# Kernel tuning notes

Measured on AMD Instinct MI355X. Metric: run time of the kernel, lower is better.

The kernel has to match this reference:

```python
import jax, jax.numpy as jnp
import numpy as np

SAMPLE_SIZE = 8192
K = 8
N_SPLATS = 1_000_000
EPS = 1e-12  # keeps sqrt grad finite on zero-distance (duplicate) pairs


def setup_inputs() -> dict:
    key = jax.random.key(0)
    k1, k2, k3 = jax.random.split(key, 3)
    means = jax.random.normal(k1, (N_SPLATS, 3), dtype=jnp.float32)
    sh0 = jax.random.normal(k2, (N_SPLATS, 1, 3), dtype=jnp.float32)
    idx = jax.random.randint(k3, (SAMPLE_SIZE,), 0, N_SPLATS, dtype=jnp.int64)
    return {"means": means, "sh0": sh0, "idx": idx}


def reference(means, sh0, idx):
    sh0 = sh0.squeeze(1)                    # [N, 3]
    sm = means[idx]                         # [S, 3] sampled positions
    ss = sh0[idx]                           # [S, 3] sampled colors
    # pairwise euclidean distances (torch.cdist, p=2): [S, S]
    sq = jnp.sum(sm * sm, axis=-1)
    d2 = sq[:, None] + sq[None, :] - 2.0 * (sm @ sm.T)
    dist = jnp.sqrt(jnp.maximum(d2, EPS))
    # k+1 smallest per row; drop self (column 0)
    _, knn_idx = jax.lax.top_k(-dist, K + 1)           # [S, K+1]
    knn_idx = knn_idx[:, 1:]                           # [S, K]
    neighbors_sh0 = ss[knn_idx]                        # [S, K, 3]
    neighbor_dist = jnp.take_along_axis(dist, knn_idx, axis=1)[..., None]  # [S, K, 1]
    weight = jnp.exp(-neighbor_dist)
    diff = ss[:, None, :] - neighbors_sh0              # [S, K, 3]
    return jnp.mean(weight * diff * diff)
```

## Files before the change

### kernel.cpp

```cpp
#include <hip/hip_runtime.h>
#include <float.h>
#include <math.h>

#define NSAMPLE 8192
#define KSEL 9
#define KNN 8
#define BLK 512
#define EPS_F 1e-12f

#define ROWS_PB 8
#define NBLOCKS (NSAMPLE / ROWS_PB)
#define RPT 8
#define LANES 64
#define KQT 16
#define CHUNK 128
#define NCHUNK (1024 / CHUNK)
#define BNDI 4
#define WCAP 32
#define BP 129
#define IDX_MASK 0x1FFFu
#define VAL_MASK 0xFFFFE000u
#define PROW 73
#define SROW 145
#define SCALE (1.0f / (float)(NSAMPLE * KNN * 3))

__device__ __forceinline__ unsigned umn(unsigned a, unsigned b) { return a < b ? a : b; }
__device__ __forceinline__ unsigned umx(unsigned a, unsigned b) { return a > b ? a : b; }

__device__ __forceinline__ void insert9(unsigned s[KSEL], unsigned x)
{
#pragma unroll
    for (int k = 0; k < KSEL - 1; ++k)
        s[k] = umx(s[k + 1], umn(x, s[k]));
    s[KSEL - 1] = umn(x, s[KSEL - 1]);
}

__device__ __forceinline__ unsigned pack_d2(float d2, int gidx)
{
    return (__float_as_uint(fmaxf(d2, 0.0f)) & VAL_MASK) | (unsigned)gidx;
}

__device__ __forceinline__ float sfl(float x)
{
    return __uint_as_float((unsigned)__builtin_amdgcn_readfirstlane(
        (int)__float_as_uint(x)));
}

__device__ __forceinline__ unsigned mbcnt64(unsigned long long m)
{
    return __builtin_amdgcn_mbcnt_hi((unsigned)(m >> 32),
           __builtin_amdgcn_mbcnt_lo((unsigned)(m & 0xFFFFFFFFull), 0u));
}

__device__ __forceinline__ void load_lds16(const float4* g, float4* l)
{
    __builtin_amdgcn_global_load_lds(
        (const __attribute__((address_space(1))) void*)g,
        (__attribute__((address_space(3))) void*)l, 16, 0, 0);
}

__global__ __launch_bounds__(256) void gather_k(
    const float* __restrict__ means, const float* __restrict__ sh0,
    const int* __restrict__ idx,
    float4* __restrict__ sm4, float4* __restrict__ ss4)
{
    int i = blockIdx.x * 256 + threadIdx.x;
    if (i >= NSAMPLE) return;
    int id = idx[i];
    const float* m = means + 3 * id;
    const float* s = sh0 + 3 * id;
    float mx = m[0], my = m[1], mz = m[2];
    sm4[i] = make_float4(mx, my, mz, fmaf(mx, mx, fmaf(my, my, mz * mz)));
    ss4[i] = make_float4(s[0], s[1], s[2], 0.0f);
}

#define QUAD(R, Q, CI)                                                        \
    {                                                                         \
        float v0 = fmaf(cX[(R) + 0], (Q).x, fmaf(cY[(R) + 0], (Q).y,          \
                   fmaf(cZ[(R) + 0], (Q).z, (Q).w)));                         \
        float v1 = fmaf(cX[(R) + 1], (Q).x, fmaf(cY[(R) + 1], (Q).y,          \
                   fmaf(cZ[(R) + 1], (Q).z, (Q).w)));                         \
        float v2 = fmaf(cX[(R) + 2], (Q).x, fmaf(cY[(R) + 2], (Q).y,          \
                   fmaf(cZ[(R) + 2], (Q).z, (Q).w)));                         \
        float v3 = fmaf(cX[(R) + 3], (Q).x, fmaf(cY[(R) + 3], (Q).y,          \
                   fmaf(cZ[(R) + 3], (Q).z, (Q).w)));                         \
        unsigned long long m0 = __ballot(v0 <= sb[(R) + 0]);                  \
        unsigned long long m1 = __ballot(v1 <= sb[(R) + 1]);                  \
        unsigned long long m2 = __ballot(v2 <= sb[(R) + 2]);                  \
        unsigned long long m3 = __ballot(v3 <= sb[(R) + 3]);                  \
        if (m0) {                                                             \
            unsigned pos = base[(R) + 0] + mbcnt64(m0);                       \
            if ((v0 <= sb[(R) + 0]) && pos < WCAP)                            \
                wl[(w * RPT + (R) + 0) * WCAP + pos] =                        \
                    pack_d2(v0 + cW[(R) + 0], (CI));                          \
            base[(R) + 0] += (unsigned)__popcll(m0);                          \
        }                                                                     \
        if (m1) {                                                             \
            unsigned pos = base[(R) + 1] + mbcnt64(m1);                       \
            if ((v1 <= sb[(R) + 1]) && pos < WCAP)                            \
                wl[(w * RPT + (R) + 1) * WCAP + pos] =                        \
                    pack_d2(v1 + cW[(R) + 1], (CI));                          \
            base[(R) + 1] += (unsigned)__popcll(m1);                          \
        }                                                                     \
        if (m2) {                                                             \
            unsigned pos = base[(R) + 2] + mbcnt64(m2);                       \
            if ((v2 <= sb[(R) + 2]) && pos < WCAP)                            \
                wl[(w * RPT + (R) + 2) * WCAP + pos] =                        \
                    pack_d2(v2 + cW[(R) + 2], (CI));                          \
            base[(R) + 2] += (unsigned)__popcll(m2);                          \
        }                                                                     \
        if (m3) {                                                             \
            unsigned pos = base[(R) + 3] + mbcnt64(m3);                       \
            if ((v3 <= sb[(R) + 3]) && pos < WCAP)                            \
                wl[(w * RPT + (R) + 3) * WCAP + pos] =                        \
                    pack_d2(v3 + cW[(R) + 3], (CI));                          \
            base[(R) + 3] += (unsigned)__popcll(m3);                          \
        }                                                                     \
    }

__global__ __launch_bounds__(BLK, 6) void main_k(
    const float4* __restrict__ sm4, const float4* __restrict__ ss4,
    float* __restrict__ partial)
{
    __shared__ float4   stg[8][2][CHUNK];
    __shared__ unsigned wl[8 * RPT * WCAP];
    __shared__ unsigned wcnt[8 * RPT];
    __shared__ unsigned bpart[ROWS_PB * BP];
    __shared__ unsigned scratch[ROWS_PB * SROW];
    __shared__ unsigned partS[ROWS_PB * PROW];
    __shared__ unsigned bnd[ROWS_PB];
    __shared__ float    red[ROWS_PB];

    const int t = threadIdx.x;
    const int lane = t & (LANES - 1);
    const int w = t >> 6;

    float cX[RPT], cY[RPT], cZ[RPT], cW[RPT];
#pragma unroll
    for (int i = 0; i < RPT; ++i) {
        float4 p = sm4[blockIdx.x * ROWS_PB + i];
        cX[i] = sfl(-2.0f * p.x);
        cY[i] = sfl(-2.0f * p.y);
        cZ[i] = sfl(-2.0f * p.z);
        cW[i] = sfl(p.w);
    }

    {
        unsigned pm[RPT];
#pragma unroll
        for (int i = 0; i < RPT; ++i) pm[i] = 0xFFFFFFFFu;
        const int b0 = w * (KQT * LANES);
        const float4* __restrict__ bp = sm4 + b0 + lane;
#pragma unroll
        for (int k = 0; k < BNDI; ++k) {
            const int ci = b0 + k * LANES + lane;
            float4 q = bp[k * LANES];
#pragma unroll
            for (int i = 0; i < RPT; ++i) {
                float s = fmaf(cX[i], q.x,
                          fmaf(cY[i], q.y, fmaf(cZ[i], q.z, q.w)));
                pm[i] = umn(pm[i], pack_d2(s + cW[i], ci));
            }
        }
#pragma unroll
        for (int i = 0; i < RPT; ++i) {
            pm[i] = umn(pm[i], (unsigned)__shfl_xor((int)pm[i], 32, 64));
            pm[i] = umn(pm[i], (unsigned)__shfl_xor((int)pm[i], 16, 64));
        }
        if (lane < 16) {
#pragma unroll
            for (int i = 0; i < RPT; ++i)
                bpart[i * BP + w * 16 + lane] = pm[i];
        }
    }
    __syncthreads();

    if (t < 128) {
        const int r1 = t & (ROWS_PB - 1);
        const int g = t >> 3;
        unsigned s[KSEL];
#pragma unroll
        for (int k = 0; k < KSEL; ++k) s[k] = 0xFFFFFFFFu;
#pragma unroll
        for (int e = 0; e < 8; ++e)
            insert9(s, bpart[r1 * BP + g * 8 + e]);
#pragma unroll
        for (int k = 0; k < KSEL; ++k)
            scratch[r1 * SROW + g * KSEL + k] = s[k];
    }
    __syncthreads();
    if (t < 64) {
        const int r1 = t & (ROWS_PB - 1);
        const int mg = t >> 3;
        unsigned m[KSEL];
#pragma unroll
        for (int k = 0; k < KSEL; ++k) m[k] = 0xFFFFFFFFu;
#pragma unroll
        for (int e = 0; e < 2 * KSEL; ++e)
            insert9(m, scratch[r1 * SROW + (2 * mg) * KSEL + e]);
#pragma unroll
        for (int k = 0; k < KSEL; ++k)
            partS[r1 * PROW + mg * KSEL + k] = m[k];
    }
    __syncthreads();
    if (t < ROWS_PB) {
        unsigned m[KSEL];
#pragma unroll
        for (int k = 0; k < KSEL; ++k) m[k] = 0xFFFFFFFFu;
#pragma unroll
        for (int e = 0; e < 8 * KSEL; ++e)
            insert9(m, partS[t * PROW + e]);
        bnd[t] = m[0];
    }
    __syncthreads();

    float sb[RPT];
#pragma unroll
    for (int i = 0; i < RPT; ++i) {
        float bfv = __uint_as_float(bnd[i] | IDX_MASK);
        float D = bfv - cW[i];
        sb[i] = sfl(D + (bfv + fabsf(D)) * 6.0e-7f + 1e-33f);
    }

    unsigned base[RPT];
#pragma unroll
    for (int i = 0; i < RPT; ++i) base[i] = 0u;

    const int s0 = w * (KQT * LANES);
    const float4* __restrict__ gsrc = sm4 + s0;

    load_lds16(gsrc + lane,      &stg[w][0][0]);
    load_lds16(gsrc + 64 + lane, &stg[w][0][64]);

#pragma unroll 1
    for (int c = 0; c < NCHUNK; ++c) {
        const float4* gn = gsrc + (c + 1) * CHUNK;
        float4* ln = &stg[w][(c + 1) & 1][0];
        load_lds16(gn + lane,      ln);
        load_lds16(gn + 64 + lane, ln + 64);

        asm volatile("s_waitcnt vmcnt(2)" ::: "memory");
        __builtin_amdgcn_sched_barrier(0);

        const float4* buf = &stg[w][c & 1][0];
        float4 q0 = buf[lane];
        float4 q1 = buf[64 + lane];
        const int ci0 = s0 + c * CHUNK + lane;
        QUAD(0, q0, ci0)
        QUAD(4, q0, ci0)
        QUAD(0, q1, ci0 + 64)
        QUAD(4, q1, ci0 + 64)
    }

    if (lane == 0) {
#pragma unroll
        for (int i = 0; i < RPT; ++i)
            wcnt[w * RPT + i] = umn(base[i], WCAP);
    }
    __syncthreads();

    if (t < 64) {
        const int r1 = t & (ROWS_PB - 1);
        const int wv = t >> 3;
        const int li = wv * RPT + r1;
        const unsigned n = wcnt[li];
        unsigned s[KSEL];
#pragma unroll
        for (int k = 0; k < KSEL; ++k) s[k] = 0xFFFFFFFFu;
        for (unsigned k = 0; k < n; ++k)
            insert9(s, wl[li * WCAP + k]);
#pragma unroll
        for (int k = 0; k < KSEL; ++k)
            partS[r1 * PROW + wv * KSEL + k] = s[k];
    }
    __syncthreads();

    if (t < ROWS_PB) {
        unsigned m[KSEL];
#pragma unroll
        for (int k = 0; k < KSEL; ++k) m[k] = 0xFFFFFFFFu;
#pragma unroll
        for (int e = 0; e < 8 * KSEL; ++e)
            insert9(m, partS[t * PROW + e]);

        const int gr = blockIdx.x * ROWS_PB + t;
        float4 pm4 = sm4[gr];
        float4 ps4 = ss4[gr];
        float acc = 0.0f;
#pragma unroll
        for (int k = 0; k < KNN; ++k) {
            int j = (int)(m[k] & IDX_MASK);
            float4 qm = sm4[j];
            float dx = pm4.x - qm.x, dy = pm4.y - qm.y, dz = pm4.z - qm.z;
            float d2 = fmaf(dx, dx, fmaf(dy, dy, dz * dz));
            float d = sqrtf(fmaxf(d2, EPS_F));
            float wgt = expf(-d);
            float4 qs = ss4[j];
            float ax = ps4.x - qs.x, ay = ps4.y - qs.y, az = ps4.z - qs.z;
            acc += wgt * (ax * ax + ay * ay + az * az);
        }
        red[t] = acc;
    }
    __syncthreads();
    if (t == 0) {
        float ssum = 0.0f;
#pragma unroll
        for (int i = 0; i < ROWS_PB; ++i) ssum += red[i];
        partial[blockIdx.x] = ssum;
    }
}

__global__ __launch_bounds__(256) void reduce_k(
    const float* __restrict__ partial, float* __restrict__ out)
{
    __shared__ float sbuf[4];
    int t = threadIdx.x;
    float v = 0.0f;
    for (int i = t; i < NBLOCKS; i += 256) v += partial[i];
    for (int off = 32; off > 0; off >>= 1) v += __shfl_down(v, off);
    if ((t & 63) == 0) sbuf[t >> 6] = v;
    __syncthreads();
    if (t == 0) {
        float s = sbuf[0] + sbuf[1] + sbuf[2] + sbuf[3];
        out[0] = s * SCALE;
    }
}

extern "C" void kernel_launch(void* const* d_in, const int* in_sizes, int n_in,
                              void* d_out, int out_size, void* d_ws, size_t ws_size,
                              hipStream_t stream)
{
    const float* means = (const float*)d_in[0];
    const float* sh0   = (const float*)d_in[1];
    const int*   idxp  = (const int*)d_in[2];

    float4* sm4 = (float4*)d_ws;
    float4* ss4 = sm4 + NSAMPLE;
    float*  partial = (float*)(ss4 + NSAMPLE);

    gather_k<<<NSAMPLE / 256, 256, 0, stream>>>(means, sh0, idxp, sm4, ss4);
    main_k<<<NBLOCKS, BLK, 0, stream>>>(sm4, ss4, partial);
    reduce_k<<<1, 256, 0, stream>>>(partial, (float*)d_out);
}
```

Baseline: 106.7 us.

## Alias shared-memory buffers into one arena to raise occupancy to 8 blocks

Replaces the separate shared arrays with one manually laid-out byte arena. The staging buffer and bpart share offset 0, and the worklist capacity per row drops from 32 to 28, so total LDS per block shrinks. Launch bounds go from 6 to 8 blocks per CU to exploit the smaller footprint. Risks are aliasing hazards if stg and bpart lifetimes overlap, more register pressure or spills under the tighter bound, and more worklist overflow with the smaller cap.

```diff
diff --git a/kernel.cpp b/kernel.cpp
--- a/kernel.cpp
+++ b/kernel.cpp
@@ -16,13 +16,21 @@
 #define CHUNK 128
 #define NCHUNK (1024 / CHUNK)
 #define BNDI 4
-#define WCAP 32
+#define WCAP 28
 #define BP 129
 #define IDX_MASK 0x1FFFu
 #define VAL_MASK 0xFFFFE000u
 #define PROW 73
 #define SROW 145
 #define SCALE (1.0f / (float)(NSAMPLE * KNN * 3))
+
+#define SMEM_BYTES 40256
+#define OFF_SCRATCH 4128
+#define OFF_PARTS   8768
+#define OFF_WL      32768
+#define OFF_WCNT    39936
+#define OFF_BND     40192
+#define OFF_RED     40224
 
 __device__ __forceinline__ unsigned umn(unsigned a, unsigned b) { return a < b ? a : b; }
 __device__ __forceinline__ unsigned umx(unsigned a, unsigned b) { return a > b ? a : b; }
@@ -118,18 +126,19 @@
         }                                                                     \
     }
 
-__global__ __launch_bounds__(BLK, 6) void main_k(
+__global__ __launch_bounds__(BLK, 8) void main_k(
     const float4* __restrict__ sm4, const float4* __restrict__ ss4,
     float* __restrict__ partial)
 {
-    __shared__ float4   stg[8][2][CHUNK];
-    __shared__ unsigned wl[8 * RPT * WCAP];
-    __shared__ unsigned wcnt[8 * RPT];
-    __shared__ unsigned bpart[ROWS_PB * BP];
-    __shared__ unsigned scratch[ROWS_PB * SROW];
-    __shared__ unsigned partS[ROWS_PB * PROW];
-    __shared__ unsigned bnd[ROWS_PB];
-    __shared__ float    red[ROWS_PB];
+    __shared__ __align__(16) unsigned char smem[SMEM_BYTES];
+    float4*   stg     = (float4*)smem;
+    unsigned* bpart   = (unsigned*)smem;
+    unsigned* scratch = (unsigned*)(smem + OFF_SCRATCH);
+    unsigned* partS   = (unsigned*)(smem + OFF_PARTS);
+    unsigned* wl      = (unsigned*)(smem + OFF_WL);
+    unsigned* wcnt    = (unsigned*)(smem + OFF_WCNT);
+    unsigned* bnd     = (unsigned*)(smem + OFF_BND);
+    float*    red     = (float*)(smem + OFF_RED);
 
     const int t = threadIdx.x;
     const int lane = t & (LANES - 1);
@@ -229,20 +238,20 @@
     const int s0 = w * (KQT * LANES);
     const float4* __restrict__ gsrc = sm4 + s0;
 
-    load_lds16(gsrc + lane,      &stg[w][0][0]);
-    load_lds16(gsrc + 64 + lane, &stg[w][0][64]);
+    load_lds16(gsrc + lane,      stg + (w * 2 + 0) * CHUNK);
+    load_lds16(gsrc + 64 + lane, stg + (w * 2 + 0) * CHUNK + 64);
 
 #pragma unroll 1
     for (int c = 0; c < NCHUNK; ++c) {
         const float4* gn = gsrc + (c + 1) * CHUNK;
-        float4* ln = &stg[w][(c + 1) & 1][0];
+        float4* ln = stg + (w * 2 + ((c + 1) & 1)) * CHUNK;
         load_lds16(gn + lane,      ln);
         load_lds16(gn + 64 + lane, ln + 64);
 
         asm volatile("s_waitcnt vmcnt(2)" ::: "memory");
         __builtin_amdgcn_sched_barrier(0);
 
-        const float4* buf = &stg[w][c & 1][0];
+        const float4* buf = stg + (w * 2 + (c & 1)) * CHUNK;
         float4 q0 = buf[lane];
         float4 q1 = buf[64 + lane];
         const int ci0 = s0 + c * CHUNK + lane;
```

Result: faster. 99.24 us (-7.0%).
